# Kernel optimization log

Hardware: AMD Instinct MI355X
Metric: run time of the kernel (lower is better)

The kernel has to match this reference:

```python
import jax, jax.numpy as jnp
import numpy as np

ROPE_BASE = 10000.0
NEG_INF = -1e30

def _apply_rope(x):
    # x: [B, H, T, D]; interleaved-pair RoPE (torchtune style), positions along axis -2.
    B, H, T, D = x.shape
    inv_freq = 1.0 / (ROPE_BASE ** (jnp.arange(0, D, 2, dtype=jnp.float32) / D))  # [D/2]
    ang = jnp.arange(T, dtype=jnp.float32)[:, None] * inv_freq[None, :]           # [T, D/2]
    cos, sin = jnp.cos(ang), jnp.sin(ang)
    x1, x2 = x[..., 0::2], x[..., 1::2]                                           # [B,H,T,D/2]
    rot = jnp.stack([x1 * cos - x2 * sin, x1 * sin + x2 * cos], axis=-1)          # [B,H,T,D/2,2]
    return rot.reshape(B, H, T, D).astype(x.dtype)

def setup_inputs() -> dict:
    key = jax.random.key(0)
    ks = jax.random.split(key, 5)
    B, T, C = 2, 2048, 1024
    s = 1.0 / np.sqrt(C)
    return {
        "x":  jax.random.normal(ks[0], (B, T, C), jnp.float32),
        "Wq": jax.random.normal(ks[1], (C, C), jnp.float32) * s,
        "bq": jnp.zeros((C,), jnp.float32),
        "Wk": jax.random.normal(ks[2], (C, C), jnp.float32) * s,
        "bk": jnp.zeros((C,), jnp.float32),
        "Wv": jax.random.normal(ks[3], (C, C), jnp.float32) * s,
        "bv": jnp.zeros((C,), jnp.float32),
        "Wo": jax.random.normal(ks[4], (C, C), jnp.float32) * s,
        "bo": jnp.zeros((C,), jnp.float32),
    }

def reference(x, Wq, bq, Wk, bk, Wv, bv, Wo, bo):
    B, T, C = x.shape
    H = 16
    D = C // H
    # QKV projections (torch Linear: x @ W.T + b), split heads -> [B, H, T, D]
    def proj(W, b):
        return (jnp.einsum('btc,oc->bto', x, W) + b).reshape(B, T, H, D).transpose(0, 2, 1, 3)
    q = _apply_rope(proj(Wq, bq))
    k = _apply_rope(proj(Wk, bk))
    v = proj(Wv, bv)
    # Causal scaled dot-product attention
    scale = 1.0 / jnp.sqrt(jnp.asarray(D, x.dtype))
    scores = jnp.einsum('bhqd,bhkd->bhqk', q, k) * scale                          # [B,H,T,T]
    causal = jnp.tril(jnp.ones((T, T), dtype=bool))
    scores = jnp.where(causal, scores, NEG_INF)
    probs = jax.nn.softmax(scores, axis=-1)
    y = jnp.einsum('bhqk,bhkd->bhqd', probs, v)                                   # [B,H,T,D]
    y = y.transpose(0, 2, 1, 3).reshape(B, T, C)
    # Output projection (dropout is identity in eval mode)
    return jnp.einsum('btc,oc->bto', y, Wo) + bo
```

## Files before the change

### kernel.cpp

```cpp
#include <hip/hip_runtime.h>

#define BB 2
#define TT 2048
#define CC 1024
#define HH 16
#define DD 64
#define KDIM 1024
#define MROWS (BB*TT)

typedef __attribute__((ext_vector_type(8))) short  frag_b16;
typedef __attribute__((ext_vector_type(4))) float  f32x4;
typedef __attribute__((ext_vector_type(4))) unsigned short us4;
typedef __attribute__((ext_vector_type(8))) unsigned short us8;
typedef __attribute__((ext_vector_type(4))) _Float16 f16x4;
typedef __attribute__((ext_vector_type(8))) _Float16 f16x8;

#define EXP2F(x) __builtin_amdgcn_exp2f(x)

__device__ __forceinline__ unsigned short f2bf(float f) {
    unsigned int u = __builtin_bit_cast(unsigned int, f);
    u += 0x7FFFu + ((u >> 16) & 1u);
    return (unsigned short)(u >> 16);
}

__device__ __forceinline__ void gl_lds16(const void* g, void* l) {
    __builtin_amdgcn_global_load_lds(
        (const __attribute__((address_space(1))) unsigned int*)g,
        (__attribute__((address_space(3))) unsigned int*)l, 16, 0, 0);
}

__global__ __launch_bounds__(256) void cvt_all(
        const float* __restrict__ x,  const float* __restrict__ w0,
        const float* __restrict__ w1, const float* __restrict__ w2,
        const float* __restrict__ w3, unsigned short* __restrict__ dst) {
    const size_t NX = (size_t)MROWS * CC;
    const size_t NW = (size_t)CC * CC;
    size_t i = ((size_t)blockIdx.x * 256 + threadIdx.x) * 4;
    const float* src; size_t off;
    if (i < NX) { src = x; off = i; }
    else {
        size_t j = i - NX;
        int t = (int)(j >> 20);
        src = (t == 0) ? w0 : (t == 1) ? w1 : (t == 2) ? w2 : w3;
        off = j & (NW - 1);
    }
    float4 f = *reinterpret_cast<const float4*>(src + off);
    us4 o;
    o.x = f2bf(f.x); o.y = f2bf(f.y); o.z = f2bf(f.z); o.w = f2bf(f.w);
    *reinterpret_cast<us4*>(dst + i) = o;
}

__global__ __launch_bounds__(256, 2) void qkv_gemm_rope(
        const unsigned short* __restrict__ X,
        const unsigned short* __restrict__ Wq,
        const unsigned short* __restrict__ Wk,
        const unsigned short* __restrict__ Wv,
        const float* __restrict__ bq, const float* __restrict__ bk,
        const float* __restrict__ bv,
        unsigned short* __restrict__ Qo,
        unsigned short* __restrict__ Ko,
        _Float16* __restrict__ VTo)
{
    const int z = blockIdx.z;
    const unsigned short* W = (z == 0) ? Wq : (z == 1) ? Wk : Wv;
    const float* bias = (z == 0) ? bq : (z == 1) ? bk : bv;

    const int tid = threadIdx.x;
    const int wave = tid >> 6;
    const int lane = tid & 63;
    const int l16 = lane & 15;
    const int quad = lane >> 4;

    const int bx = blockIdx.x * 128;
    const int by = blockIdx.y * 128;
    const int row0 = bx + (wave >> 1) * 64;
    const int col0 = by + (wave & 1) * 64;

    __shared__ __align__(16) char smem[65536];
    unsigned short* Xa0 = (unsigned short*)smem;
    unsigned short* Wb0 = (unsigned short*)(smem + 32768);
    _Float16 (*Vl)[64][72] = (_Float16(*)[64][72])smem;

    f32x4 acc[4][4] = {};

    int srow[4]; int scol[4];
#pragma unroll
    for (int i = 0; i < 4; ++i) {
        int n = tid + 256 * i;
        srow[i] = n >> 3;
        scol[i] = ((n & 7) ^ (srow[i] & 7)) * 8;
    }

#pragma unroll
    for (int i = 0; i < 4; ++i) {
        int n = tid + 256 * i;
        gl_lds16(X + (size_t)(bx + srow[i]) * KDIM + scol[i], Xa0 + n * 8);
        gl_lds16(W + (size_t)(by + srow[i]) * KDIM + scol[i], Wb0 + n * 8);
    }

    const int ar = (wave >> 1) * 64;
    const int bc = (wave & 1) * 64;

#pragma unroll 1
    for (int step = 0; step < 16; ++step) {
        __syncthreads();
        const int bsel = step & 1;
        if (step + 1 < 16) {
            const int kk = (step + 1) * 64;
            const int bo_ = (bsel ^ 1) * 8192;
#pragma unroll
            for (int i = 0; i < 4; ++i) {
                int n = tid + 256 * i;
                gl_lds16(X + (size_t)(bx + srow[i]) * KDIM + kk + scol[i],
                         Xa0 + bo_ + n * 8);
                gl_lds16(W + (size_t)(by + srow[i]) * KDIM + kk + scol[i],
                         Wb0 + bo_ + n * 8);
            }
        }

        frag_b16 a[4][2], b[4][2];
#pragma unroll
        for (int r = 0; r < 4; ++r) {
            int row = ar + r * 16 + l16;
#pragma unroll
            for (int kh = 0; kh < 2; ++kh) {
                int c = (kh * 4 + quad) ^ (row & 7);
                a[r][kh] = *reinterpret_cast<const frag_b16*>(
                    Xa0 + bsel * 8192 + row * 64 + c * 8);
            }
        }
#pragma unroll
        for (int cc = 0; cc < 4; ++cc) {
            int row = bc + cc * 16 + l16;
#pragma unroll
            for (int kh = 0; kh < 2; ++kh) {
                int c = (kh * 4 + quad) ^ (row & 7);
                b[cc][kh] = *reinterpret_cast<const frag_b16*>(
                    Wb0 + bsel * 8192 + row * 64 + c * 8);
            }
        }
#pragma unroll
        for (int r = 0; r < 4; ++r)
#pragma unroll
            for (int c = 0; c < 4; ++c) {
                acc[r][c] = __builtin_amdgcn_mfma_f32_16x16x32_bf16(a[r][0], b[c][0], acc[r][c], 0, 0, 0);
                acc[r][c] = __builtin_amdgcn_mfma_f32_16x16x32_bf16(a[r][1], b[c][1], acc[r][c], 0, 0, 0);
            }
    }

    __syncthreads();

    if (z == 2) {
#pragma unroll
        for (int r = 0; r < 4; ++r)
#pragma unroll
            for (int c = 0; c < 4; ++c) {
                f16x4 pk;
#pragma unroll
                for (int g = 0; g < 4; ++g)
                    pk[g] = (_Float16)(acc[r][c][g] + bias[col0 + c * 16 + l16]);
                *reinterpret_cast<f16x4*>(&Vl[wave][c * 16 + l16][r * 16 + quad * 4]) = pk;
            }
        const int b_ = row0 >> 11;
        const int t_base = row0 & (TT - 1);
        const int h = col0 >> 6;
        const int dl = lane >> 3;
        const int t8 = (lane & 7) * 8;
        __builtin_amdgcn_s_waitcnt(0);
#pragma unroll
        for (int i = 0; i < 8; ++i) {
            int d = i * 8 + dl;
            f16x8 v = *reinterpret_cast<const f16x8*>(&Vl[wave][d][t8]);
            *reinterpret_cast<f16x8*>(
                &VTo[((size_t)(b_ * HH + h) * DD + d) * TT + t_base + t8]) = v;
        }
    } else {
        const float qsc = (z == 0) ? 0.180336888f : 1.0f;
        unsigned short* dst = (z == 0) ? Qo : Ko;
        const int b_ = row0 >> 11;
        const int tq0 = (row0 & (TT - 1)) + quad * 4;
#pragma unroll
        for (int c = 0; c < 4; ++c) {
            const int o = col0 + c * 16 + l16;
            const int h = o >> 6, d = o & (DD - 1);
            const float inv = __expf(-(float)(d & ~1) * (9.210340371976184f / (float)DD));
            float cs0, sn0, cs1, sn1, cs16, sn16;
            __sincosf((float)tq0 * inv, &sn0, &cs0);
            __sincosf(inv, &sn1, &cs1);
            __sincosf(16.f * inv, &sn16, &cs16);
            float cr = cs0, sr = sn0;
#pragma unroll
            for (int r = 0; r < 4; ++r) {
                float cg = cr, sg = sr;
#pragma unroll
                for (int g = 0; g < 4; ++g) {
                    int n = row0 + r * 16 + quad * 4 + g;
                    int t = n & (TT - 1);
                    float v = acc[r][c][g] + bias[o];
                    float pv = __shfl_xor(v, 1);
                    float outv = (d & 1) ? (pv * sg + v * cg) : (v * cg - pv * sg);
                    dst[((size_t)(b_ * HH + h) * TT + t) * DD + d] = f2bf(outv * qsc);
                    float cn = cg * cs1 - sg * sn1;
                    sg = sg * cs1 + cg * sn1;
                    cg = cn;
                }
                float crn = cr * cs16 - sr * sn16;
                sr = sr * cs16 + cr * sn16;
                cr = crn;
            }
        }
    }
}

__global__ __launch_bounds__(256, 2) void attn(
        const unsigned short* __restrict__ Q,
        const unsigned short* __restrict__ K,
        const _Float16* __restrict__ VT,
        unsigned short* __restrict__ Y)
{
    const int b1d = blockIdx.x;
    const int bh = (b1d & 7) * 4 + ((b1d >> 3) & 3);
    const int pair = b1d >> 5;
    const int tid = threadIdx.x;
    const int w = tid >> 6;
    const int lane = tid & 63;
    const int l16 = lane & 15;
    const int quad = lane >> 4;

    const unsigned short* Qp = Q + (size_t)bh * TT * DD;
    const unsigned short* Kp = K + (size_t)bh * TT * DD;
    const _Float16* Vp = VT + (size_t)bh * DD * TT;

    __shared__ unsigned short Kl[2][128][64];
    __shared__ _Float16 Vl[2][64][128];
    __shared__ unsigned short Ylds[4][16][72];

    const int sw = (l16 & 7);
    const int b_ = bh >> 4, h = bh & (HH - 1);

    f16x4 ones;
    ones[0] = ones[1] = ones[2] = ones[3] = (_Float16)1.0f;

#pragma unroll 1
    for (int seg = 0; seg < 2; ++seg) {
        const int qblk = seg ? (31 - pair) : pair;
        const int q0 = qblk * 64;
        const int q = q0 + w * 16 + l16;

        frag_b16 bq[2];
#pragma unroll
        for (int dk = 0; dk < 2; ++dk)
            bq[dk] = *reinterpret_cast<const frag_b16*>(
                Qp + (size_t)q * DD + dk * 32 + quad * 8);

        f32x4 yacc[4] = {};
        f32x4 lsum = {};

        const int ntiles = (qblk >> 1) + 1;

#pragma unroll
        for (int i = 0; i < 4; ++i) {
            int n = tid + 256 * i;
            int kr = n >> 3,  kc = ((n & 7)  ^ (kr & 7)) * 8;
            int vr = n >> 4,  vc = ((n & 15) ^ (vr & 7)) * 8;
            gl_lds16(Kp + (size_t)kr * DD + kc, (unsigned short*)&Kl[0][0][0] + n * 8);
            gl_lds16(Vp + (size_t)vr * TT + vc, (_Float16*)&Vl[0][0][0] + n * 8);
        }

#pragma unroll 1
        for (int it = 0; it < ntiles; ++it) {
            __syncthreads();
            const int bsel = it & 1;
            if (it + 1 < ntiles) {
                const int jn = (it + 1) * 128;
                const int bn = bsel ^ 1;
#pragma unroll
                for (int i = 0; i < 4; ++i) {
                    int n = tid + 256 * i;
                    int kr = n >> 3,  kc = ((n & 7)  ^ (kr & 7)) * 8;
                    int vr = n >> 4,  vc = ((n & 15) ^ (vr & 7)) * 8;
                    gl_lds16(Kp + (size_t)(jn + kr) * DD + kc,
                             (unsigned short*)&Kl[bn][0][0] + n * 8);
                    gl_lds16(Vp + (size_t)vr * TT + jn + vc,
                             (_Float16*)&Vl[bn][0][0] + n * 8);
                }
            }
            const int j0 = it * 128;

            f32x4 s[8];
#pragma unroll
            for (int mt = 0; mt < 8; ++mt) {
                frag_b16 ak0 = *reinterpret_cast<const frag_b16*>(
                    &Kl[bsel][mt * 16 + l16][(quad ^ sw) * 8]);
                frag_b16 ak1 = *reinterpret_cast<const frag_b16*>(
                    &Kl[bsel][mt * 16 + l16][((4 + quad) ^ sw) * 8]);
                f32x4 t = {};
                t = __builtin_amdgcn_mfma_f32_16x16x32_bf16(ak0, bq[0], t, 0, 0, 0);
                t = __builtin_amdgcn_mfma_f32_16x16x32_bf16(ak1, bq[1], t, 0, 0, 0);
                s[mt] = t;
            }

            if (it == ntiles - 1) {
#pragma unroll
                for (int mt = 0; mt < 8; ++mt)
#pragma unroll
                    for (int g = 0; g < 4; ++g) {
                        int key = j0 + mt * 16 + quad * 4 + g;
                        if (key > q) s[mt][g] = -1e30f;
                    }
            }

            f16x4 pb[8];
#pragma unroll
            for (int mt = 0; mt < 8; ++mt)
#pragma unroll
                for (int g = 0; g < 4; ++g)
                    pb[mt][g] = (_Float16)EXP2F(s[mt][g] - 11.0f);

#pragma unroll
            for (int kt = 0; kt < 8; ++kt)
                lsum = __builtin_amdgcn_mfma_f32_16x16x16f16(ones, pb[kt], lsum, 0, 0, 0);

#pragma unroll
            for (int dt = 0; dt < 4; ++dt) {
                f32x4 ya = yacc[dt];
#pragma unroll
                for (int kt = 0; kt < 8; ++kt) {
                    int colp = (kt * 2 + (quad >> 1)) ^ sw;
                    f16x4 av = *reinterpret_cast<const f16x4*>(
                        &Vl[bsel][dt * 16 + l16][colp * 8 + (quad & 1) * 4]);
                    ya = __builtin_amdgcn_mfma_f32_16x16x16f16(av, pb[kt], ya, 0, 0, 0);
                }
                yacc[dt] = ya;
            }
        }

        __syncthreads();

        float rl = 1.f / lsum[0];
#pragma unroll
        for (int dt = 0; dt < 4; ++dt)
#pragma unroll
            for (int g = 0; g < 4; ++g)
                Ylds[w][l16][dt * 16 + quad * 4 + g] = f2bf(yacc[dt][g] * rl);

#pragma unroll
        for (int i = 0; i < 2; ++i) {
            int idx = i * 64 + lane;
            int r = idx >> 3, c8 = (idx & 7) * 8;
            us8 v = *reinterpret_cast<const us8*>(&Ylds[w][r][c8]);
            *reinterpret_cast<us8*>(
                &Y[(size_t)(b_ * TT + q0 + w * 16 + r) * CC + h * DD + c8]) = v;
        }
    }
}

__global__ __launch_bounds__(256, 2) void out_gemm(
        const unsigned short* __restrict__ Y,
        const unsigned short* __restrict__ Wo,
        const float* __restrict__ bo,
        float* __restrict__ out)
{
    const int tid = threadIdx.x;
    const int wave = tid >> 6;
    const int lane = tid & 63;
    const int l16 = lane & 15;
    const int quad = lane >> 4;

    const int bx = blockIdx.x * 128;
    const int by = blockIdx.y * 128;
    const int row0 = bx + (wave >> 1) * 64;
    const int col0 = by + (wave & 1) * 64;

    __shared__ __align__(16) char smem[65536];
    unsigned short* Xa0 = (unsigned short*)smem;
    unsigned short* Wb0 = (unsigned short*)(smem + 32768);

    f32x4 acc[4][4] = {};

    int srow[4]; int scol[4];
#pragma unroll
    for (int i = 0; i < 4; ++i) {
        int n = tid + 256 * i;
        srow[i] = n >> 3;
        scol[i] = ((n & 7) ^ (srow[i] & 7)) * 8;
    }

#pragma unroll
    for (int i = 0; i < 4; ++i) {
        int n = tid + 256 * i;
        gl_lds16(Y  + (size_t)(bx + srow[i]) * KDIM + scol[i], Xa0 + n * 8);
        gl_lds16(Wo + (size_t)(by + srow[i]) * KDIM + scol[i], Wb0 + n * 8);
    }

    const int ar = (wave >> 1) * 64;
    const int bc = (wave & 1) * 64;

#pragma unroll 1
    for (int step = 0; step < 16; ++step) {
        __syncthreads();
        const int bsel = step & 1;
        if (step + 1 < 16) {
            const int kk = (step + 1) * 64;
            const int bo_ = (bsel ^ 1) * 8192;
#pragma unroll
            for (int i = 0; i < 4; ++i) {
                int n = tid + 256 * i;
                gl_lds16(Y  + (size_t)(bx + srow[i]) * KDIM + kk + scol[i],
                         Xa0 + bo_ + n * 8);
                gl_lds16(Wo + (size_t)(by + srow[i]) * KDIM + kk + scol[i],
                         Wb0 + bo_ + n * 8);
            }
        }

        frag_b16 a[4][2], b[4][2];
#pragma unroll
        for (int r = 0; r < 4; ++r) {
            int row = ar + r * 16 + l16;
#pragma unroll
            for (int kh = 0; kh < 2; ++kh) {
                int c = (kh * 4 + quad) ^ (row & 7);
                a[r][kh] = *reinterpret_cast<const frag_b16*>(
                    Xa0 + bsel * 8192 + row * 64 + c * 8);
            }
        }
#pragma unroll
        for (int cc = 0; cc < 4; ++cc) {
            int row = bc + cc * 16 + l16;
#pragma unroll
            for (int kh = 0; kh < 2; ++kh) {
                int c = (kh * 4 + quad) ^ (row & 7);
                b[cc][kh] = *reinterpret_cast<const frag_b16*>(
                    Wb0 + bsel * 8192 + row * 64 + c * 8);
            }
        }
#pragma unroll
        for (int r = 0; r < 4; ++r)
#pragma unroll
            for (int c = 0; c < 4; ++c) {
                acc[r][c] = __builtin_amdgcn_mfma_f32_16x16x32_bf16(a[r][0], b[c][0], acc[r][c], 0, 0, 0);
                acc[r][c] = __builtin_amdgcn_mfma_f32_16x16x32_bf16(a[r][1], b[c][1], acc[r][c], 0, 0, 0);
            }
    }

#pragma unroll
    for (int r = 0; r < 4; ++r)
#pragma unroll
        for (int c = 0; c < 4; ++c)
#pragma unroll
            for (int g = 0; g < 4; ++g) {
                int n = row0 + r * 16 + quad * 4 + g;
                int o = col0 + c * 16 + l16;
                out[(size_t)n * CC + o] = acc[r][c][g] + bo[o];
            }
}

extern "C" void kernel_launch(void* const* d_in, const int* in_sizes, int n_in,
                              void* d_out, int out_size, void* d_ws, size_t ws_size,
                              hipStream_t stream) {
    const float* x  = (const float*)d_in[0];
    const float* Wq = (const float*)d_in[1];
    const float* bq = (const float*)d_in[2];
    const float* Wk = (const float*)d_in[3];
    const float* bk = (const float*)d_in[4];
    const float* Wv = (const float*)d_in[5];
    const float* bv = (const float*)d_in[6];
    const float* Wo = (const float*)d_in[7];
    const float* bo = (const float*)d_in[8];
    float* out = (float*)d_out;

    unsigned short* ws = (unsigned short*)d_ws;
    const size_t NX = (size_t)MROWS * CC;
    const size_t NW = (size_t)CC * CC;
    unsigned short* xb  = ws;
    unsigned short* wqb = xb  + NX;
    unsigned short* wkb = wqb + NW;
    unsigned short* wvb = wkb + NW;
    unsigned short* wob = wvb + NW;
    unsigned short* Qr  = wob + NW;
    unsigned short* Kr  = Qr  + NX;
    _Float16*       VTb = (_Float16*)(Kr + NX);
    unsigned short* Yb  = (unsigned short*)(VTb + NX);

    const size_t NALL = NX + 4 * NW;
    cvt_all<<<dim3((unsigned)(NALL / 1024)), 256, 0, stream>>>(x, Wq, Wk, Wv, Wo, xb);

    qkv_gemm_rope<<<dim3(MROWS / 128, CC / 128, 3), 256, 0, stream>>>(
        xb, wqb, wkb, wvb, bq, bk, bv, Qr, Kr, VTb);

    attn<<<dim3(512), 256, 0, stream>>>(Qr, Kr, VTb, Yb);

    out_gemm<<<dim3(MROWS / 128, CC / 128), 256, 0, stream>>>(Yb, wob, bo, out);
}
```

Measured before the change: 168.4 us.

## Enlarge QKV GEMM tile to 256x256 with 8 waves and interleaved prefetch

Rewrites the QKV projection GEMM to use 256x256 block tiles with 512 threads (8 waves, 128x64 per wave) and 128KB of LDS. It splits each k-tile into four quarter-steps that interleave global-to-LDS prefetch, register double-buffering of B fragments, and MFMA bursts under raised wave priority, using partial vmcnt waits and raw barriers. The goal is more operand reuse per LDS byte and better overlap of loads with compute. In exchange, the grid shrinks to 16x4x3=192 blocks, which may underfill the CUs, and register and LDS pressure rise.

```diff
diff --git a/kernel.cpp b/kernel.cpp
--- a/kernel.cpp
+++ b/kernel.cpp
@@ -50,7 +50,7 @@
     *reinterpret_cast<us4*>(dst + i) = o;
 }
 
-__global__ __launch_bounds__(256, 2) void qkv_gemm_rope(
+__global__ __launch_bounds__(512, 2) void qkv_gemm_rope(
         const unsigned short* __restrict__ X,
         const unsigned short* __restrict__ Wq,
         const unsigned short* __restrict__ Wk,
@@ -66,122 +66,158 @@
     const float* bias = (z == 0) ? bq : (z == 1) ? bk : bv;
 
     const int tid = threadIdx.x;
-    const int wave = tid >> 6;
+    const int w = tid >> 6;
     const int lane = tid & 63;
     const int l16 = lane & 15;
     const int quad = lane >> 4;
-
-    const int bx = blockIdx.x * 128;
-    const int by = blockIdx.y * 128;
-    const int row0 = bx + (wave >> 1) * 64;
-    const int col0 = by + (wave & 1) * 64;
-
-    __shared__ __align__(16) char smem[65536];
-    unsigned short* Xa0 = (unsigned short*)smem;
-    unsigned short* Wb0 = (unsigned short*)(smem + 32768);
+    const int wm = w >> 2;
+    const int wn = w & 3;
+
+    const int bx = blockIdx.x * 256;
+    const int by = blockIdx.y * 256;
+    const int rowbase = bx + wm * 128;
+    const int colbase = by + wn * 64;
+
+    __shared__ __align__(16) char smem[131072];
+    unsigned short* Ab = (unsigned short*)smem;
+    unsigned short* Bb = (unsigned short*)(smem + 65536);
     _Float16 (*Vl)[64][72] = (_Float16(*)[64][72])smem;
 
-    f32x4 acc[4][4] = {};
-
-    int srow[4]; int scol[4];
-#pragma unroll
-    for (int i = 0; i < 4; ++i) {
-        int n = tid + 256 * i;
-        srow[i] = n >> 3;
-        scol[i] = ((n & 7) ^ (srow[i] & 7)) * 8;
-    }
-
-#pragma unroll
-    for (int i = 0; i < 4; ++i) {
-        int n = tid + 256 * i;
-        gl_lds16(X + (size_t)(bx + srow[i]) * KDIM + scol[i], Xa0 + n * 8);
-        gl_lds16(W + (size_t)(by + srow[i]) * KDIM + scol[i], Wb0 + n * 8);
-    }
-
-    const int ar = (wave >> 1) * 64;
-    const int bc = (wave & 1) * 64;
+    f32x4 acc[8][4] = {};
+
+    const int nB0 = (tid & 255) + ((tid >> 8) << 9);
+
+    {
+        const int an[4] = { tid, tid + 512, tid + 1024, tid + 1536 };
+        const int bn[4] = { nB0, nB0 + 256, nB0 + 1024, nB0 + 1280 };
+#pragma unroll
+        for (int i = 0; i < 4; ++i) {
+            int r = an[i] >> 3, cc_ = ((an[i] & 7) ^ (r & 7)) * 8;
+            gl_lds16(X + (size_t)(bx + r) * KDIM + cc_, Ab + an[i] * 8);
+            r = bn[i] >> 3; cc_ = ((bn[i] & 7) ^ (r & 7)) * 8;
+            gl_lds16(W + (size_t)(by + r) * KDIM + cc_, Bb + bn[i] * 8);
+        }
+    }
+    asm volatile("s_waitcnt vmcnt(0)" ::: "memory");
+    __builtin_amdgcn_s_barrier();
+
+    frag_b16 bC[4][2], bN[4][2];
+#pragma unroll
+    for (int c = 0; c < 4; ++c) {
+        const int row = wn * 64 + c * 16 + l16;
+        const unsigned short* Br = Bb + row * 64;
+#pragma unroll
+        for (int kh = 0; kh < 2; ++kh) {
+            const int sl = (kh * 4 + quad) ^ (row & 7);
+            bC[c][kh] = *reinterpret_cast<const frag_b16*>(Br + sl * 8);
+        }
+    }
+
+    auto ktile = [&](int t, int bsel, frag_b16 (&bA)[4][2], frag_b16 (&bNx)[4][2]) {
+        const bool pre = (t + 1 < 16);
+        const int kk = (t + 1) * 64;
+        const unsigned short* Ac = Ab + bsel * 16384;
+        unsigned short* An = Ab + (bsel ^ 1) * 16384;
+        unsigned short* Bn = Bb + (bsel ^ 1) * 16384;
+#pragma unroll
+        for (int q = 0; q < 4; ++q) {
+            frag_b16 a[2][2];
+#pragma unroll
+            for (int m = 0; m < 2; ++m) {
+                const int row = wm * 128 + q * 32 + m * 16 + l16;
+                const unsigned short* Ar = Ac + row * 64;
+#pragma unroll
+                for (int kh = 0; kh < 2; ++kh) {
+                    const int sl = (kh * 4 + quad) ^ (row & 7);
+                    a[m][kh] = *reinterpret_cast<const frag_b16*>(Ar + sl * 8);
+                }
+            }
+            if (q >= 2 && pre) {
+#pragma unroll
+                for (int hh = 0; hh < 2; ++hh) {
+                    const int c = (q - 2) * 2 + hh;
+                    const int row = wn * 64 + c * 16 + l16;
+                    const unsigned short* Br = Bn + row * 64;
+#pragma unroll
+                    for (int kh = 0; kh < 2; ++kh) {
+                        const int sl = (kh * 4 + quad) ^ (row & 7);
+                        bNx[c][kh] = *reinterpret_cast<const frag_b16*>(Br + sl * 8);
+                    }
+                }
+            }
+            if (pre) {
+                int n0, n1; const unsigned short* G; unsigned short* L; int g0;
+                if (q == 0)      { n0 = nB0;        n1 = nB0 + 1024; G = W; L = Bn; g0 = by; }
+                else if (q == 1) { n0 = nB0 + 256;  n1 = nB0 + 1280; G = W; L = Bn; g0 = by; }
+                else if (q == 2) { n0 = tid;        n1 = tid + 1024; G = X; L = An; g0 = bx; }
+                else             { n0 = tid + 512;  n1 = tid + 1536; G = X; L = An; g0 = bx; }
+                {   int r = n0 >> 3, cc_ = ((n0 & 7) ^ (r & 7)) * 8;
+                    gl_lds16(G + (size_t)(g0 + r) * KDIM + kk + cc_, L + n0 * 8); }
+                {   int r = n1 >> 3, cc_ = ((n1 & 7) ^ (r & 7)) * 8;
+                    gl_lds16(G + (size_t)(g0 + r) * KDIM + kk + cc_, L + n1 * 8); }
+            }
+            __builtin_amdgcn_s_barrier();
+            __builtin_amdgcn_s_setprio(1);
+#pragma unroll
+            for (int m = 0; m < 2; ++m)
+#pragma unroll
+                for (int c = 0; c < 4; ++c) {
+                    acc[q * 2 + m][c] = __builtin_amdgcn_mfma_f32_16x16x32_bf16(
+                        a[m][0], bA[c][0], acc[q * 2 + m][c], 0, 0, 0);
+                    acc[q * 2 + m][c] = __builtin_amdgcn_mfma_f32_16x16x32_bf16(
+                        a[m][1], bA[c][1], acc[q * 2 + m][c], 0, 0, 0);
+                }
+            __builtin_amdgcn_s_setprio(0);
+            asm volatile("s_waitcnt vmcnt(2)" ::: "memory");
+            __builtin_amdgcn_s_barrier();
+        }
+    };
 
 #pragma unroll 1
-    for (int step = 0; step < 16; ++step) {
-        __syncthreads();
-        const int bsel = step & 1;
-        if (step + 1 < 16) {
-            const int kk = (step + 1) * 64;
-            const int bo_ = (bsel ^ 1) * 8192;
-#pragma unroll
-            for (int i = 0; i < 4; ++i) {
-                int n = tid + 256 * i;
-                gl_lds16(X + (size_t)(bx + srow[i]) * KDIM + kk + scol[i],
-                         Xa0 + bo_ + n * 8);
-                gl_lds16(W + (size_t)(by + srow[i]) * KDIM + kk + scol[i],
-                         Wb0 + bo_ + n * 8);
-            }
-        }
-
-        frag_b16 a[4][2], b[4][2];
-#pragma unroll
-        for (int r = 0; r < 4; ++r) {
-            int row = ar + r * 16 + l16;
-#pragma unroll
-            for (int kh = 0; kh < 2; ++kh) {
-                int c = (kh * 4 + quad) ^ (row & 7);
-                a[r][kh] = *reinterpret_cast<const frag_b16*>(
-                    Xa0 + bsel * 8192 + row * 64 + c * 8);
-            }
-        }
-#pragma unroll
-        for (int cc = 0; cc < 4; ++cc) {
-            int row = bc + cc * 16 + l16;
-#pragma unroll
-            for (int kh = 0; kh < 2; ++kh) {
-                int c = (kh * 4 + quad) ^ (row & 7);
-                b[cc][kh] = *reinterpret_cast<const frag_b16*>(
-                    Wb0 + bsel * 8192 + row * 64 + c * 8);
-            }
-        }
-#pragma unroll
-        for (int r = 0; r < 4; ++r)
-#pragma unroll
-            for (int c = 0; c < 4; ++c) {
-                acc[r][c] = __builtin_amdgcn_mfma_f32_16x16x32_bf16(a[r][0], b[c][0], acc[r][c], 0, 0, 0);
-                acc[r][c] = __builtin_amdgcn_mfma_f32_16x16x32_bf16(a[r][1], b[c][1], acc[r][c], 0, 0, 0);
-            }
-    }
-
-    __syncthreads();
+    for (int tt = 0; tt < 8; ++tt) {
+        ktile(2 * tt,     0, bC, bN);
+        ktile(2 * tt + 1, 1, bN, bC);
+    }
 
     if (z == 2) {
-#pragma unroll
-        for (int r = 0; r < 4; ++r)
-#pragma unroll
-            for (int c = 0; c < 4; ++c) {
-                f16x4 pk;
-#pragma unroll
-                for (int g = 0; g < 4; ++g)
-                    pk[g] = (_Float16)(acc[r][c][g] + bias[col0 + c * 16 + l16]);
-                *reinterpret_cast<f16x4*>(&Vl[wave][c * 16 + l16][r * 16 + quad * 4]) = pk;
-            }
-        const int b_ = row0 >> 11;
-        const int t_base = row0 & (TT - 1);
-        const int h = col0 >> 6;
+        const int b_ = rowbase >> 11;
+        const int h  = colbase >> 6;
         const int dl = lane >> 3;
         const int t8 = (lane & 7) * 8;
-        __builtin_amdgcn_s_waitcnt(0);
-#pragma unroll
-        for (int i = 0; i < 8; ++i) {
-            int d = i * 8 + dl;
-            f16x8 v = *reinterpret_cast<const f16x8*>(&Vl[wave][d][t8]);
-            *reinterpret_cast<f16x8*>(
-                &VTo[((size_t)(b_ * HH + h) * DD + d) * TT + t_base + t8]) = v;
+#pragma unroll
+        for (int hp = 0; hp < 2; ++hp) {
+#pragma unroll
+            for (int r4 = 0; r4 < 4; ++r4) {
+                const int r = hp * 4 + r4;
+#pragma unroll
+                for (int c = 0; c < 4; ++c) {
+                    f16x4 pk;
+#pragma unroll
+                    for (int g = 0; g < 4; ++g)
+                        pk[g] = (_Float16)(acc[r][c][g] + bias[colbase + c * 16 + l16]);
+                    *reinterpret_cast<f16x4*>(
+                        &Vl[w][c * 16 + l16][r4 * 16 + quad * 4]) = pk;
+                }
+            }
+            __builtin_amdgcn_s_waitcnt(0);
+#pragma unroll
+            for (int i = 0; i < 8; ++i) {
+                const int d = i * 8 + dl;
+                f16x8 v = *reinterpret_cast<const f16x8*>(&Vl[w][d][t8]);
+                *reinterpret_cast<f16x8*>(
+                    &VTo[((size_t)(b_ * HH + h) * DD + d) * TT
+                         + (rowbase & (TT - 1)) + hp * 64 + t8]) = v;
+            }
+            __builtin_amdgcn_s_waitcnt(0);
         }
     } else {
         const float qsc = (z == 0) ? 0.180336888f : 1.0f;
         unsigned short* dst = (z == 0) ? Qo : Ko;
-        const int b_ = row0 >> 11;
-        const int tq0 = (row0 & (TT - 1)) + quad * 4;
+        const int b_ = rowbase >> 11;
+        const int tq0 = (rowbase & (TT - 1)) + quad * 4;
 #pragma unroll
         for (int c = 0; c < 4; ++c) {
-            const int o = col0 + c * 16 + l16;
+            const int o = colbase + c * 16 + l16;
             const int h = o >> 6, d = o & (DD - 1);
             const float inv = __expf(-(float)(d & ~1) * (9.210340371976184f / (float)DD));
             float cs0, sn0, cs1, sn1, cs16, sn16;
@@ -190,11 +226,11 @@
             __sincosf(16.f * inv, &sn16, &cs16);
             float cr = cs0, sr = sn0;
 #pragma unroll
-            for (int r = 0; r < 4; ++r) {
+            for (int r = 0; r < 8; ++r) {
                 float cg = cr, sg = sr;
 #pragma unroll
                 for (int g = 0; g < 4; ++g) {
-                    int n = row0 + r * 16 + quad * 4 + g;
+                    int n = rowbase + r * 16 + quad * 4 + g;
                     int t = n & (TT - 1);
                     float v = acc[r][c][g] + bias[o];
                     float pv = __shfl_xor(v, 1);
@@ -485,7 +521,7 @@
     const size_t NALL = NX + 4 * NW;
     cvt_all<<<dim3((unsigned)(NALL / 1024)), 256, 0, stream>>>(x, Wq, Wk, Wv, Wo, xb);
 
-    qkv_gemm_rope<<<dim3(MROWS / 128, CC / 128, 3), 256, 0, stream>>>(
+    qkv_gemm_rope<<<dim3(MROWS / 256, CC / 256, 3), 512, 0, stream>>>(
         xb, wqb, wkb, wvb, bq, bk, bv, Qr, Kr, VTb);
 
     attn<<<dim3(512), 256, 0, stream>>>(Qr, Kr, VTb, Yb);
```

Result: slower. 180.7 us (+7.3%).
